# Performance work log

Hardware: AMD Instinct MI355X
Metric: run time of the kernel (lower is better)

## Reference

```python
import jax, jax.numpy as jnp
import numpy as np

NUM_BINS = 36
MIN_ACTIVATION = 0.1
PENALTY_WEIGHT = 1.0


def setup_inputs() -> dict:
    key = jax.random.key(0)
    k1, k2 = jax.random.split(key)
    mask = jax.random.uniform(k1, (64, 1, 640, 640), dtype=jnp.float32)
    bbox = jax.random.uniform(k2, (64, 4), dtype=jnp.float32)
    return {"mask": mask, "bbox": bbox}


def reference(mask, bbox):
    B, _, H, W = mask.shape
    nb = NUM_BINS
    # pixel-space bbox centers
    cx = bbox[:, 0] * W  # (B,)
    cy = bbox[:, 1] * H  # (B,)
    x = jnp.arange(W, dtype=jnp.float32)
    y = jnp.arange(H, dtype=jnp.float32)
    # (B, H, W) offsets from each sample's center
    dx = x[None, None, :] - cx[:, None, None]
    dy = y[None, :, None] - cy[:, None, None]
    angles = jnp.arctan2(dy, dx)  # (B, H, W) in [-pi, pi]
    binf = (angles + jnp.pi) / (2.0 * jnp.pi) * nb
    bins = jnp.clip(binf.astype(jnp.int32), 0, nb - 1)  # (B, H, W)
    # fused per-(sample, bin) segment mean via a single scatter-add pass
    seg = (bins + jnp.arange(B, dtype=jnp.int32)[:, None, None] * nb).reshape(-1)
    m = mask[:, 0].reshape(-1)
    sums = jax.ops.segment_sum(m, seg, num_segments=B * nb)
    cnts = jax.ops.segment_sum(jnp.ones_like(m), seg, num_segments=B * nb)
    act = jnp.where(cnts > 0, sums / jnp.maximum(cnts, 1.0), 0.0).reshape(B, nb)
    under = (act < MIN_ACTIVATION).astype(jnp.float32)
    penalty_per_sample = under.sum(axis=1) / nb
    return PENALTY_WEIGHT * penalty_per_sample.mean()
```

## Files before the change

### kernel.cpp

```cpp
#include <hip/hip_runtime.h>
#include <math.h>

#define NB 36
#define W 640
#define H 640
#define NSAMP 64
#define RPB 40
#define BPS 16
#define FIX_SCALE 4194304.0f
#define INV_FIX (1.0f/4194304.0f)
#define CNT_SHIFT 44
#define AMB 1e-6

__device__ __forceinline__ int bin_slow(int x, int y, double cxd, double cyd) {
    const double PI_D    = 3.141592653589793;
    const double TWOPI_D = 6.283185307179586;
    double t  = (atan2((double)y - cyd, (double)x - cxd) + PI_D) / TWOPI_D;
    double bd = t * 36.0;
    int k = (int)bd;
    k = k < 0 ? 0 : k;
    return k > NB - 1 ? NB - 1 : k;
}

__global__ void acl_setup(unsigned long long* __restrict__ ws) {
    int i = blockIdx.x * 256 + threadIdx.x;
    if (i < NSAMP * NB) ws[i] = 0ull;
    if (blockIdx.x == 0 && threadIdx.x < NB) {
        double* tbl = (double*)(ws + NSAMP * NB);
        int m = threadIdx.x;
        double t = 0.0;
        if (m != 18) {
            double th = (double)(m - 18) * (3.141592653589793 / 18.0);
            t = cos(th) / sin(th);
        }
        tbl[m] = t;
    }
}

#define SCAN_STEP(x, ctrl, rmask)                                             \
    x += (unsigned)__builtin_amdgcn_update_dpp(0, (int)(x), (ctrl), (rmask),  \
                                               0xf, false)

__global__ __launch_bounds__(256) void acl_main(const float* __restrict__ mask,
                                                const float* __restrict__ bbox,
                                                unsigned long long* __restrict__ ws) {
    __shared__ int A_l[RPB][18];
    __shared__ int sgn_l[RPB];
    __shared__ __align__(16) unsigned srow[4][2][768];
    __shared__ unsigned long long lbin[NB];

    const int tid = threadIdx.x;
    const int b   = blockIdx.x >> 4;
    const int rg  = blockIdx.x & (BPS - 1);
    const int y0  = rg * RPB;

    if (tid < NB) lbin[tid] = 0ull;
    if (tid < RPB) A_l[tid][17] = W - 1;

    const double cxd = (double)bbox[b * 4 + 0] * 640.0;
    const double cyd = (double)bbox[b * 4 + 1] * 640.0;
    const double* tbl = (const double*)(ws + NSAMP * NB);

    for (int task = tid; task < RPB * 17; task += 256) {
        const int rl = task / 17, mi = task % 17;
        const int y  = y0 + rl;
        const double dy = (double)y - cyd;
        int i, a;
        if (dy == 0.0) {
            if (mi == 0) sgn_l[rl] = 0;
            i = mi;
            a = (mi == 0) ? ((int)ceil(cxd) - 1) : (W - 1);
        } else {
            const bool dp = (dy > 0.0);
            if (mi == 0) sgn_l[rl] = dp ? 1 : -1;
            const int m = dp ? (19 + mi) : (1 + mi);
            double x = cxd + dy * tbl[m];
            x = fmin(fmax(x, -2.0), 642.0);
            double g  = x + 2.0;
            int    gi = (int)g;
            double fr = g - (double)gi;
            int v = dp ? (gi - 2)
                       : (gi - 1);
            if (fr < AMB || fr > 1.0 - AMB) {
                int xa = (int)(x + 2.5) - 2;
                if (xa >= 0 && xa <= W - 1) {
                    int kb = bin_slow(xa, y, cxd, cyd);
                    if (dp) v = (kb >= m) ? xa : xa - 1;
                    else    v = (kb >= m) ? xa : xa + 1;
                }
            }
            if (dp) { i = 16 - mi; a = v; }
            else    { i = mi;      a = v - 1; }
        }
        a = a < -1 ? -1 : (a > W - 1 ? W - 1 : a);
        A_l[rl][i] = a;
    }
    __syncthreads();

    const int wid = tid >> 6, lane = tid & 63;
    const float* rowbase = mask + (size_t)b * (W * H) + (size_t)y0 * W;

    unsigned long long accPs = 0ull, accNs = 0ull;
    unsigned accPc = 0u, accNc = 0u;

    const float4* rp = (const float4*)(rowbase + (size_t)wid * W);
    float4 c0 = rp[lane];
    float4 c1 = rp[lane + 64];
    float4 c2 = (lane < 32) ? rp[lane + 128] : make_float4(0.f, 0.f, 0.f, 0.f);

    for (int j = 0; j < 10; j++) {
        const int rl = wid + 4 * j;
        float4 n0, n1, n2;
        if (j < 9) {
            const float4* np = (const float4*)(rowbase + (size_t)(rl + 4) * W);
            n0 = np[lane];
            n1 = np[lane + 64];
            n2 = (lane < 32) ? np[lane + 128] : make_float4(0.f, 0.f, 0.f, 0.f);
        }

        const int buf = j & 1;
        unsigned carry = 0u;
        #pragma unroll
        for (int s = 0; s < 3; s++) {
            const float4 v = (s == 0) ? c0 : (s == 1) ? c1 : c2;
            const unsigned q0 = __float2uint_rn(v.x * FIX_SCALE);
            const unsigned q1 = __float2uint_rn(v.y * FIX_SCALE);
            const unsigned q2 = __float2uint_rn(v.z * FIX_SCALE);
            const unsigned q3 = __float2uint_rn(v.w * FIX_SCALE);
            const unsigned p0 = q0, p1 = p0 + q1, p2 = p1 + q2, p3 = p2 + q3;

            unsigned x = p3;
            SCAN_STEP(x, 0x111, 0xf);
            SCAN_STEP(x, 0x112, 0xf);
            SCAN_STEP(x, 0x114, 0xf);
            SCAN_STEP(x, 0x118, 0xf);
            SCAN_STEP(x, 0x142, 0xa);
            SCAN_STEP(x, 0x143, 0xc);
            const unsigned base = carry + (x - p3);
            uint4 wv;
            wv.x = base + p0; wv.y = base + p1; wv.z = base + p2; wv.w = base + p3;
            *((uint4*)&srow[wid][buf][s * 256 + lane * 4]) = wv;
            carry += (unsigned)__builtin_amdgcn_readlane((int)x, 63);
        }

        if (lane < 18) {
            const int aR = A_l[rl][lane];
            const int aL = (lane == 0) ? -1 : A_l[rl][lane - 1];
            const int cnt = aR - aL;
            if (cnt > 0) {
                const unsigned sR = srow[wid][buf][aR];
                const unsigned sL = (aL >= 0) ? srow[wid][buf][aL] : 0u;
                const unsigned seg = sR - sL;
                const int sg = sgn_l[rl];
                if (sg > 0)      { accPc += (unsigned)cnt; accPs += seg; }
                else if (sg < 0) { accNc += (unsigned)cnt; accNs += seg; }
                else atomicAdd(&lbin[(lane == 0) ? 35 : 18],
                               ((unsigned long long)cnt << CNT_SHIFT)
                               + (unsigned long long)seg);
            }
        }
        if (j < 9) { c0 = n0; c1 = n1; c2 = n2; }
    }

    if (lane < 18) {
        if (accPc) atomicAdd(&lbin[35 - lane],
                             ((unsigned long long)accPc << CNT_SHIFT) + accPs);
        if (accNc) atomicAdd(&lbin[lane],
                             ((unsigned long long)accNc << CNT_SHIFT) + accNs);
    }
    __syncthreads();
    if (tid < NB) {
        const unsigned long long v = lbin[tid];
        if (v) atomicAdd(&ws[b * NB + tid], v);
    }
}

__global__ __launch_bounds__(256) void acl_final(const unsigned long long* __restrict__ ws,
                                                 float* __restrict__ out) {
    __shared__ unsigned long long h[NSAMP * NB];
    __shared__ float s[NSAMP];
    const int tid = threadIdx.x;
    for (int i = tid; i < NSAMP * NB; i += 256) h[i] = ws[i];
    __syncthreads();
    if (tid < NSAMP) {
        int nunder = 0;
        for (int k = 0; k < NB; k++) {
            const unsigned long long v = h[tid * NB + k];
            const unsigned long long cnt = v >> CNT_SHIFT;
            const float sum = (float)(v & ((1ull << CNT_SHIFT) - 1)) * INV_FIX;
            const float act = (cnt != 0ull) ? (sum / (float)cnt) : 0.0f;
            if (act < 0.1f) nunder++;
        }
        s[tid] = (float)nunder / 36.0f;
    }
    __syncthreads();
    if (tid == 0) {
        float acc = 0.0f;
        for (int i = 0; i < NSAMP; i++) acc += s[i];
        out[0] = acc / 64.0f;
    }
}

extern "C" void kernel_launch(void* const* d_in, const int* in_sizes, int n_in,
                              void* d_out, int out_size, void* d_ws, size_t ws_size,
                              hipStream_t stream) {
    const float* mask = (const float*)d_in[0];
    const float* bbox = (const float*)d_in[1];
    unsigned long long* ws = (unsigned long long*)d_ws;

    acl_setup<<<dim3((NSAMP * NB + 255) / 256), dim3(256), 0, stream>>>(ws);
    acl_main<<<dim3(NSAMP * BPS), dim3(256), 0, stream>>>(mask, bbox, ws);
    acl_final<<<dim3(1), dim3(256), 0, stream>>>(ws, (float*)d_out);
}
```

Measured before the change: 35.87 us.

## Drop setup kernel, write per-block partials, prefetch two rows ahead

Removes the setup kernel by moving the cotangent table into constant memory and having each block write its per-bin partials to a dedicated workspace slot instead of atomically adding into a zeroed buffer. The final kernel now reduces the 16 partials per sample in parallel across 256 threads. The row loop prefetches two rows ahead and uses a single shared-memory row buffer per wave. This saves a kernel launch and the global atomics, at the cost of more global reads in the single-block final kernel.

```diff
diff --git a/kernel.cpp b/kernel.cpp
--- a/kernel.cpp
+++ b/kernel.cpp
@@ -7,10 +7,30 @@
 #define NSAMP 64
 #define RPB 40
 #define BPS 16
+#define NBLK (NSAMP * BPS)
+#define PSTRIDE 40
 #define FIX_SCALE 4194304.0f
 #define INV_FIX (1.0f/4194304.0f)
 #define CNT_SHIFT 44
+#define SUM_MASK ((1ull << CNT_SHIFT) - 1)
 #define AMB 1e-6
+
+__device__ __constant__ double COT[36] = {
+    0.0,
+    5.6712818196177095,  2.7474774194546223,  1.7320508075688773,
+    1.1917535925942100,  0.8390996311772800,  0.5773502691896258,
+    0.3639702342662024,  0.1763269807084650,  0.0,
+    -0.1763269807084650, -0.3639702342662024, -0.5773502691896258,
+    -0.8390996311772800, -1.1917535925942100, -1.7320508075688773,
+    -2.7474774194546223, -5.6712818196177095,
+    0.0,
+    5.6712818196177095,  2.7474774194546223,  1.7320508075688773,
+    1.1917535925942100,  0.8390996311772800,  0.5773502691896258,
+    0.3639702342662024,  0.1763269807084650,  0.0,
+    -0.1763269807084650, -0.3639702342662024, -0.5773502691896258,
+    -0.8390996311772800, -1.1917535925942100, -1.7320508075688773,
+    -2.7474774194546223, -5.6712818196177095
+};
 
 __device__ __forceinline__ int bin_slow(int x, int y, double cxd, double cyd) {
     const double PI_D    = 3.141592653589793;
@@ -22,21 +42,6 @@
     return k > NB - 1 ? NB - 1 : k;
 }
 
-__global__ void acl_setup(unsigned long long* __restrict__ ws) {
-    int i = blockIdx.x * 256 + threadIdx.x;
-    if (i < NSAMP * NB) ws[i] = 0ull;
-    if (blockIdx.x == 0 && threadIdx.x < NB) {
-        double* tbl = (double*)(ws + NSAMP * NB);
-        int m = threadIdx.x;
-        double t = 0.0;
-        if (m != 18) {
-            double th = (double)(m - 18) * (3.141592653589793 / 18.0);
-            t = cos(th) / sin(th);
-        }
-        tbl[m] = t;
-    }
-}
-
 #define SCAN_STEP(x, ctrl, rmask)                                             \
     x += (unsigned)__builtin_amdgcn_update_dpp(0, (int)(x), (ctrl), (rmask),  \
                                                0xf, false)
@@ -46,7 +51,7 @@
                                                 unsigned long long* __restrict__ ws) {
     __shared__ int A_l[RPB][18];
     __shared__ int sgn_l[RPB];
-    __shared__ __align__(16) unsigned srow[4][2][768];
+    __shared__ __align__(16) unsigned srow[4][768];
     __shared__ unsigned long long lbin[NB];
 
     const int tid = threadIdx.x;
@@ -59,7 +64,6 @@
 
     const double cxd = (double)bbox[b * 4 + 0] * 640.0;
     const double cyd = (double)bbox[b * 4 + 1] * 640.0;
-    const double* tbl = (const double*)(ws + NSAMP * NB);
 
     for (int task = tid; task < RPB * 17; task += 256) {
         const int rl = task / 17, mi = task % 17;
@@ -74,7 +78,7 @@
             const bool dp = (dy > 0.0);
             if (mi == 0) sgn_l[rl] = dp ? 1 : -1;
             const int m = dp ? (19 + mi) : (1 + mi);
-            double x = cxd + dy * tbl[m];
+            double x = cxd + dy * COT[m];
             x = fmin(fmax(x, -2.0), 642.0);
             double g  = x + 2.0;
             int    gi = (int)g;
@@ -103,26 +107,28 @@
     unsigned long long accPs = 0ull, accNs = 0ull;
     unsigned accPc = 0u, accNc = 0u;
 
-    const float4* rp = (const float4*)(rowbase + (size_t)wid * W);
-    float4 c0 = rp[lane];
-    float4 c1 = rp[lane + 64];
-    float4 c2 = (lane < 32) ? rp[lane + 128] : make_float4(0.f, 0.f, 0.f, 0.f);
+    const float4 z4 = make_float4(0.f, 0.f, 0.f, 0.f);
+    const float4* rpA = (const float4*)(rowbase + (size_t)wid * W);
+    float4 a0 = rpA[lane], a1 = rpA[lane + 64];
+    float4 a2 = (lane < 32) ? rpA[lane + 128] : z4;
+    const float4* rpB = (const float4*)(rowbase + (size_t)(wid + 4) * W);
+    float4 b0 = rpB[lane], b1 = rpB[lane + 64];
+    float4 b2 = (lane < 32) ? rpB[lane + 128] : z4;
 
     for (int j = 0; j < 10; j++) {
         const int rl = wid + 4 * j;
         float4 n0, n1, n2;
-        if (j < 9) {
-            const float4* np = (const float4*)(rowbase + (size_t)(rl + 4) * W);
+        if (j < 8) {
+            const float4* np = (const float4*)(rowbase + (size_t)(rl + 8) * W);
             n0 = np[lane];
             n1 = np[lane + 64];
-            n2 = (lane < 32) ? np[lane + 128] : make_float4(0.f, 0.f, 0.f, 0.f);
-        }
-
-        const int buf = j & 1;
+            n2 = (lane < 32) ? np[lane + 128] : z4;
+        }
+
         unsigned carry = 0u;
         #pragma unroll
         for (int s = 0; s < 3; s++) {
-            const float4 v = (s == 0) ? c0 : (s == 1) ? c1 : c2;
+            const float4 v = (s == 0) ? a0 : (s == 1) ? a1 : a2;
             const unsigned q0 = __float2uint_rn(v.x * FIX_SCALE);
             const unsigned q1 = __float2uint_rn(v.y * FIX_SCALE);
             const unsigned q2 = __float2uint_rn(v.z * FIX_SCALE);
@@ -139,7 +145,7 @@
             const unsigned base = carry + (x - p3);
             uint4 wv;
             wv.x = base + p0; wv.y = base + p1; wv.z = base + p2; wv.w = base + p3;
-            *((uint4*)&srow[wid][buf][s * 256 + lane * 4]) = wv;
+            *((uint4*)&srow[wid][s * 256 + lane * 4]) = wv;
             carry += (unsigned)__builtin_amdgcn_readlane((int)x, 63);
         }
 
@@ -148,8 +154,8 @@
             const int aL = (lane == 0) ? -1 : A_l[rl][lane - 1];
             const int cnt = aR - aL;
             if (cnt > 0) {
-                const unsigned sR = srow[wid][buf][aR];
-                const unsigned sL = (aL >= 0) ? srow[wid][buf][aL] : 0u;
+                const unsigned sR = srow[wid][aR];
+                const unsigned sL = (aL >= 0) ? srow[wid][aL] : 0u;
                 const unsigned seg = sR - sL;
                 const int sg = sgn_l[rl];
                 if (sg > 0)      { accPc += (unsigned)cnt; accPs += seg; }
@@ -159,7 +165,8 @@
                                + (unsigned long long)seg);
             }
         }
-        if (j < 9) { c0 = n0; c1 = n1; c2 = n2; }
+        a0 = b0; a1 = b1; a2 = b2;
+        b0 = n0; b1 = n1; b2 = n2;
     }
 
     if (lane < 18) {
@@ -169,29 +176,35 @@
                              ((unsigned long long)accNc << CNT_SHIFT) + accNs);
     }
     __syncthreads();
-    if (tid < NB) {
-        const unsigned long long v = lbin[tid];
-        if (v) atomicAdd(&ws[b * NB + tid], v);
-    }
+    if (tid < NB)
+        ws[(size_t)blockIdx.x * PSTRIDE + tid] = lbin[tid];
 }
 
 __global__ __launch_bounds__(256) void acl_final(const unsigned long long* __restrict__ ws,
                                                  float* __restrict__ out) {
-    __shared__ unsigned long long h[NSAMP * NB];
+    __shared__ unsigned nund[256];
     __shared__ float s[NSAMP];
     const int tid = threadIdx.x;
-    for (int i = tid; i < NSAMP * NB; i += 256) h[i] = ws[i];
+    const int b = tid >> 2, q = tid & 3;
+    unsigned cu = 0;
+    #pragma unroll
+    for (int kk = 0; kk < 9; kk++) {
+        const int k = q * 9 + kk;
+        unsigned long long tot = 0ull;
+        #pragma unroll
+        for (int g = 0; g < BPS; g++)
+            tot += ws[(size_t)(b * BPS + g) * PSTRIDE + k];
+        const unsigned long long cnt = tot >> CNT_SHIFT;
+        const float sum = (float)(tot & SUM_MASK) * INV_FIX;
+        const float act = (cnt != 0ull) ? (sum / (float)cnt) : 0.0f;
+        if (act < 0.1f) cu++;
+    }
+    nund[tid] = cu;
     __syncthreads();
     if (tid < NSAMP) {
-        int nunder = 0;
-        for (int k = 0; k < NB; k++) {
-            const unsigned long long v = h[tid * NB + k];
-            const unsigned long long cnt = v >> CNT_SHIFT;
-            const float sum = (float)(v & ((1ull << CNT_SHIFT) - 1)) * INV_FIX;
-            const float act = (cnt != 0ull) ? (sum / (float)cnt) : 0.0f;
-            if (act < 0.1f) nunder++;
-        }
-        s[tid] = (float)nunder / 36.0f;
+        const unsigned n = nund[4 * tid] + nund[4 * tid + 1]
+                         + nund[4 * tid + 2] + nund[4 * tid + 3];
+        s[tid] = (float)n / 36.0f;
     }
     __syncthreads();
     if (tid == 0) {
@@ -208,7 +221,6 @@
     const float* bbox = (const float*)d_in[1];
     unsigned long long* ws = (unsigned long long*)d_ws;
 
-    acl_setup<<<dim3((NSAMP * NB + 255) / 256), dim3(256), 0, stream>>>(ws);
-    acl_main<<<dim3(NSAMP * BPS), dim3(256), 0, stream>>>(mask, bbox, ws);
+    acl_main<<<dim3(NBLK), dim3(256), 0, stream>>>(mask, bbox, ws);
     acl_final<<<dim3(1), dim3(256), 0, stream>>>(ws, (float*)d_out);
 }
```

Measured after the change: 38.64 us. 1.08x slower.
